# Performance work log

Hardware: AMD Instinct MI355X
Metric: run time of the kernel (lower is better)

The kernel has to match this reference:

```python
import jax, jax.numpy as jnp
import numpy as np

N_NODES = 50000
N_EDGES = 800000
IN_CH = 512
HID = 512


def setup_inputs() -> dict:
    key = jax.random.key(0)
    ks = jax.random.split(key, 8)
    x = jax.random.normal(ks[0], (N_NODES, IN_CH), dtype=jnp.float32)
    edge_index = jax.random.randint(ks[1], (2, N_EDGES), 0, N_NODES, dtype=jnp.int64)
    s_in = 1.0 / np.sqrt(IN_CH)
    s_h = 1.0 / np.sqrt(HID)
    W1 = jax.random.uniform(ks[2], (IN_CH, HID), jnp.float32, -s_in, s_in)
    b1 = jnp.zeros((HID,), jnp.float32)
    W2 = jax.random.uniform(ks[3], (HID, HID), jnp.float32, -s_h, s_h)
    b2 = jnp.zeros((HID,), jnp.float32)
    Wo = jax.random.uniform(ks[4], (HID, 1), jnp.float32, -s_h, s_h)
    bo = jnp.zeros((1,), jnp.float32)
    return {"x": x, "edge_index": edge_index, "W1": W1, "b1": b1,
            "W2": W2, "b2": b2, "Wo": Wo, "bo": bo}


def _gcn_norm(edge_index, n):
    # add self-loops, compute symmetric normalization deg^{-1/2} per edge
    loop = jnp.arange(n, dtype=edge_index.dtype)
    src = jnp.concatenate([edge_index[0], loop])  # [E+N]
    dst = jnp.concatenate([edge_index[1], loop])
    deg = jax.ops.segment_sum(jnp.ones_like(dst, dtype=jnp.float32), dst,
                              num_segments=n)
    dinv = jnp.where(deg > 0, jax.lax.rsqrt(jnp.maximum(deg, 1.0)), 0.0)
    norm = dinv[src] * dinv[dst]  # [E+N]
    return src, dst, norm


def _gcn_conv(h, src, dst, norm, W, b, n):
    h = h @ W                          # [N, H] dense GEMM first (PyG order)
    msg = h[src] * norm[:, None]       # gather + per-edge scale
    out = jax.ops.segment_sum(msg, dst, num_segments=n)  # scatter-add
    return out + b


def reference(x, edge_index, W1, b1, W2, b2, Wo, bo):
    n = x.shape[0]
    src, dst, norm = _gcn_norm(edge_index, n)
    h = jax.nn.relu(_gcn_conv(x, src, dst, norm, W1, b1, n))
    h = jax.nn.relu(_gcn_conv(h, src, dst, norm, W2, b2, n))
    logits = (h @ Wo + bo)[:, 0]       # [N]
    return jax.nn.softmax(logits, axis=0)
```

## Files before the change

### kernel.cpp

```cpp
#include <hip/hip_runtime.h>

#define NN 50000
#define NP 50176
#define NE 800000
#define CH 512
#define NB 196
#define PB_TRANS 2048
#define PB_DEG 782
#define PB_PERM 6
#define SMB 49
#define GB1 (4 * (NP / 128))
#define BKB ((NE / 2 + 255) / 256)

typedef __bf16 bf16x8 __attribute__((ext_vector_type(8)));
typedef float f32x4 __attribute__((ext_vector_type(4)));
typedef float f32x2 __attribute__((ext_vector_type(2)));
typedef unsigned short u16x8 __attribute__((ext_vector_type(8)));

static __device__ __forceinline__ unsigned short f2b(float f){
  unsigned u = __builtin_bit_cast(unsigned, f);
  u = (u + 0x7fffu + ((u >> 16) & 1u)) >> 16;
  return (unsigned short)u;
}
static __device__ __forceinline__ float b2f(unsigned short h){
  unsigned u = ((unsigned)h) << 16;
  return __builtin_bit_cast(float, u);
}
static __device__ __forceinline__ float rdlane_f(float v, int l){
  return __builtin_bit_cast(float, __builtin_amdgcn_readlane(__builtin_bit_cast(int, v), l));
}
static __device__ __forceinline__ unsigned pack2(float f0, float f1){
  unsigned u0 = __builtin_bit_cast(unsigned, f0) + 0x8000u;
  unsigned u1 = __builtin_bit_cast(unsigned, f1) + 0x8000u;
  return __builtin_amdgcn_perm(u1, u0, 0x07060302u);
}
static __device__ __forceinline__ int lam(int p){
  return (p & ~63) | (((p & 3) << 4) + ((p & 63) >> 2));
}

__global__ void k_prep(const float* __restrict__ W1, const float* __restrict__ W2,
                       unsigned short* __restrict__ W1t, unsigned short* __restrict__ W2t,
                       const int* __restrict__ ei, int* __restrict__ deg,
                       int* __restrict__ rank,
                       const float* __restrict__ b1, const float* __restrict__ b2,
                       const float* __restrict__ Wo, float* __restrict__ b1p,
                       float* __restrict__ b2p, float* __restrict__ Wop){
  const int b = blockIdx.x, t = threadIdx.x;
  if (b < PB_TRANS){
    int idx = (b & 1023) * 256 + t;
    int n = idx >> 9, p = idx & (CH - 1);
    if (b < 1024)
      W1t[n * CH + p] = f2b(W1[p * CH + n]);
    else
      W2t[n * CH + p] = f2b(W2[lam(p) * CH + n]);
  } else if (b < PB_TRANS + PB_DEG){
    int e4 = ((b - PB_TRANS) * 256 + t) * 4;
    if (e4 < NE){
      int4 d = *(const int4*)(ei + NE + e4);
      int4 r;
      r.x = atomicAdd(&deg[d.x], 1);
      r.y = atomicAdd(&deg[d.y], 1);
      r.z = atomicAdd(&deg[d.z], 1);
      r.w = atomicAdd(&deg[d.w], 1);
      *(int4*)(rank + e4) = r;
    }
  } else {
    int idx = (b - PB_TRANS - PB_DEG) * 256 + t;
    int which = idx >> 9, p = idx & (CH - 1);
    int l = lam(p);
    if (which == 0) b1p[p] = b1[l];
    else if (which == 1) b2p[p] = b2[l];
    else Wop[p] = Wo[l];
  }
}

__global__ void k_blocksum(const int* __restrict__ deg, int* __restrict__ bsum){
  __shared__ int sh[4];
  const int t = threadIdx.x;
  int i = blockIdx.x * 256 + t;
  int v = (i < NN) ? deg[i] : 0;
  #pragma unroll
  for (int off = 32; off > 0; off >>= 1) v += __shfl_down(v, off, 64);
  if ((t & 63) == 0) sh[t >> 6] = v;
  __syncthreads();
  if (t == 0) bsum[blockIdx.x] = sh[0] + sh[1] + sh[2] + sh[3];
}

__global__ void k_scatter(const int* __restrict__ deg, const int* __restrict__ bsum,
                          int* __restrict__ row_ptr, float* __restrict__ dinv){
  __shared__ int sh[256];
  __shared__ int base;
  const int t = threadIdx.x;
  int bv = (t < NB) ? bsum[t] : 0;
  sh[t] = bv; __syncthreads();
  for (int d = 1; d < 256; d <<= 1){
    int add = (t >= d) ? sh[t - d] : 0;
    __syncthreads();
    sh[t] += add;
    __syncthreads();
  }
  if (t == (int)blockIdx.x) base = sh[t] - bv;
  if (blockIdx.x == 0 && t == 255) row_ptr[NN] = sh[255];
  __syncthreads();
  const int boff0 = base;
  int i = blockIdx.x * 256 + t;
  int d0 = (i < NN) ? deg[i] : 0;
  sh[t] = d0; __syncthreads();
  for (int dd = 1; dd < 256; dd <<= 1){
    int add = (t >= dd) ? sh[t - dd] : 0;
    __syncthreads();
    sh[t] += add;
    __syncthreads();
  }
  if (i < NN){
    row_ptr[i] = sh[t] - d0 + boff0;
    dinv[i] = rsqrtf((float)d0 + 1.0f);
  }
}

template<bool CVT>
static __device__ __forceinline__ void gemm_body(
    const int bx, const int t,
    const void* __restrict__ Av, const unsigned short* __restrict__ Bt,
    unsigned char* __restrict__ C,
    unsigned short (&As)[2][8192], unsigned short (&Bs)[2][8192]){
  const int wave = t >> 6, lane = t & 63;
  const int quad = lane >> 4, l15 = lane & 15;
  const int mw = (wave & 1) * 64;
  const int nw = (wave >> 1) * 64;
  const int g = bx >> 5, rem = bx & 31;
  const int rt = g * 8 + (rem & 7);
  const int rowBase = rt * 128;
  const int nBase = (rem >> 3) * 128;

  const int lr = lane >> 2;
  const int lcs = (((lane & 3) ^ ((lr >> 1) & 3)) * 8);
  const int lr8 = lane >> 3;
  const int lc8 = lane & 7;
  const unsigned short* Bg0 = Bt + (size_t)(nBase + wave * 32 + lr) * CH + lcs;
  const int boff = wave * 1024;
  const float* X = (const float*)Av;
  const unsigned short* Ag0 = (const unsigned short*)Av;
  if (!CVT) Ag0 += (size_t)(rowBase + wave * 32 + lr) * CH + lcs;
  const int aoff = wave * 1024;

  int arow[4]; size_t asrc[4];
  int wswz = 0;
  if (CVT){
    #pragma unroll
    for (int q=0;q<4;q++){
      arow[q] = wave * 32 + q * 8 + lr8;
      int gr = rowBase + arow[q];
      if (gr >= NN) gr = 0;
      asrc[q] = (size_t)gr * CH + lc8 * 4;
    }
    wswz = (lc8 * 4) ^ ((lr8 & 6) << 2);
  }
  const int rsw = (l15 & 6) << 2;

  f32x4 acc[4][4];
  #pragma unroll
  for (int i=0;i<4;i++)
    #pragma unroll
    for (int j=0;j<4;j++) acc[i][j] = 0;

  float4 apre[2][4];

  if (CVT){
    #pragma unroll
    for (int p=0;p<2;p++)
      #pragma unroll
      for (int q=0;q<4;q++) apre[p][q] = *(const float4*)(X + asrc[q] + p*32);
    #pragma unroll
    for (int p=0;p<2;p++)
      #pragma unroll
      for (int q=0;q<4;q++){
        uint2 pk; pk.x = pack2(apre[p][q].x, apre[p][q].y);
        pk.y = pack2(apre[p][q].z, apre[p][q].w);
        *(uint2*)&As[0][p*4096 + arow[q]*32 + wswz] = pk;
      }
  } else {
    #pragma unroll
    for (int p=0;p<2;p++)
      #pragma unroll
      for (int gg=0;gg<2;gg++)
        __builtin_amdgcn_global_load_lds(
          (const __attribute__((address_space(1))) void*)(Ag0 + (size_t)gg*16*CH + p*32),
          (__attribute__((address_space(3))) void*)(&As[0][p*4096 + aoff + gg*512]), 16, 0, 0);
  }
  #pragma unroll
  for (int p=0;p<2;p++)
    #pragma unroll
    for (int gg=0;gg<2;gg++)
      __builtin_amdgcn_global_load_lds(
        (const __attribute__((address_space(1))) void*)(Bg0 + (size_t)gg*16*CH + p*32),
        (__attribute__((address_space(3))) void*)(&Bs[0][p*4096 + boff + gg*512]), 16, 0, 0);

  for (int it = 0; it < 8; it++){
    const int cur = it & 1, nxt = cur ^ 1;
    __syncthreads();
    if (it < 7){
      const int kb = (it + 1) * 64;
      if (CVT){
        #pragma unroll
        for (int p=0;p<2;p++)
          #pragma unroll
          for (int q=0;q<4;q++) apre[p][q] = *(const float4*)(X + asrc[q] + kb + p*32);
      } else {
        #pragma unroll
        for (int p=0;p<2;p++)
          #pragma unroll
          for (int gg=0;gg<2;gg++)
            __builtin_amdgcn_global_load_lds(
              (const __attribute__((address_space(1))) void*)(Ag0 + (size_t)gg*16*CH + kb + p*32),
              (__attribute__((address_space(3))) void*)(&As[nxt][p*4096 + aoff + gg*512]), 16, 0, 0);
      }
      #pragma unroll
      for (int p=0;p<2;p++)
        #pragma unroll
        for (int gg=0;gg<2;gg++)
          __builtin_amdgcn_global_load_lds(
            (const __attribute__((address_space(1))) void*)(Bg0 + (size_t)gg*16*CH + kb + p*32),
            (__attribute__((address_space(3))) void*)(&Bs[nxt][p*4096 + boff + gg*512]), 16, 0, 0);
    }

    #pragma unroll
    for (int ks=0;ks<2;ks++){
      bf16x8 af[4], bfr[4];
      #pragma unroll
      for (int i=0;i<4;i++)
        af[i] = __builtin_bit_cast(bf16x8,
                *(const u16x8*)&As[cur][ks*4096 + (mw + i*16 + l15)*32 + (quad*8 ^ rsw)]);
      #pragma unroll
      for (int j=0;j<4;j++)
        bfr[j] = __builtin_bit_cast(bf16x8,
                *(const u16x8*)&Bs[cur][ks*4096 + (nw + j*16 + l15)*32 + (quad*8 ^ rsw)]);
      #pragma unroll
      for (int i=0;i<4;i++)
        #pragma unroll
        for (int j=0;j<4;j++)
          acc[i][j] = __builtin_amdgcn_mfma_f32_16x16x32_bf16(af[i], bfr[j], acc[i][j], 0, 0, 0);
    }

    if (CVT && it < 7){
      #pragma unroll
      for (int p=0;p<2;p++)
        #pragma unroll
        for (int q=0;q<4;q++){
          uint2 pk; pk.x = pack2(apre[p][q].x, apre[p][q].y);
          pk.y = pack2(apre[p][q].z, apre[p][q].w);
          *(uint2*)&As[nxt][p*4096 + arow[q]*32 + wswz] = pk;
        }
    }
  }

  #pragma unroll
  for (int i=0;i<4;i++){
    #pragma unroll
    for (int r=0;r<4;r++){
      int row = rowBase + mw + i*16 + quad*4 + r;
      int w0 = 0;
      w0 = __builtin_amdgcn_cvt_pk_fp8_f32(acc[i][0][r], acc[i][1][r], w0, false);
      w0 = __builtin_amdgcn_cvt_pk_fp8_f32(acc[i][2][r], acc[i][3][r], w0, true);
      *(unsigned*)(C + (size_t)row * CH + nBase + nw + l15*4) = (unsigned)w0;
    }
  }
}

__launch_bounds__(256, 2)
__global__ void k_g1bkt(const float* __restrict__ x, const unsigned short* __restrict__ W1t,
                        unsigned char* __restrict__ C,
                        const int* __restrict__ ei, const int* __restrict__ row_ptr,
                        const int* __restrict__ rank, int* __restrict__ csr_src){
  __shared__ __align__(16) unsigned short As[2][8192];
  __shared__ __align__(16) unsigned short Bs[2][8192];
  const int b = blockIdx.x;
  if (b < GB1){
    gemm_body<true>(b, threadIdx.x, x, W1t, C, As, Bs);
  } else {
    int e2 = ((b - GB1) * 256 + threadIdx.x) * 2;
    if (e2 < NE){
      int2 src = *(const int2*)(ei + e2);
      int2 dst = *(const int2*)(ei + NE + e2);
      int2 rk  = *(const int2*)(rank + e2);
      csr_src[row_ptr[dst.x] + rk.x] = src.x;
      csr_src[row_ptr[dst.y] + rk.y] = src.y;
    }
  }
}

__launch_bounds__(256, 2)
__global__ void k_gemm2(const unsigned short* __restrict__ A,
                        const unsigned short* __restrict__ Bt,
                        unsigned char* __restrict__ C){
  __shared__ __align__(16) unsigned short As[2][8192];
  __shared__ __align__(16) unsigned short Bs[2][8192];
  gemm_body<false>(blockIdx.x, threadIdx.x, A, Bt, C, As, Bs);
}

template<bool HEAD>
__launch_bounds__(256)
__global__ void k_agg(const unsigned char* __restrict__ h, const int* __restrict__ row_ptr,
                      const int* __restrict__ csr_src, const float* __restrict__ dinv,
                      const float* __restrict__ bias, unsigned short* __restrict__ out,
                      const float* __restrict__ Wo, const float* __restrict__ bo,
                      float* __restrict__ logits){
  const int node = blockIdx.x * 4 + (threadIdx.x >> 6);
  const int lane = threadIdx.x & 63;
  float acc[8];
  #pragma unroll
  for (int k=0;k<8;k++) acc[k] = 0.f;
  const int rp = row_ptr[node], re = row_ptr[node + 1];
  for (int base = rp; base < re; base += 64){
    int cnt = re - base; if (cnt > 64) cnt = 64;
    int s = 0; float w = 0.f;
    if (base + lane < re){ s = csr_src[base + lane]; w = dinv[s]; }
    int j = 0;
    for (; j + 8 <= cnt; j += 8){
      int ss[8]; float ww[8]; uint2 hv[8];
      #pragma unroll
      for (int u=0;u<8;u++){
        ss[u] = __builtin_amdgcn_readlane(s, j + u);
        ww[u] = rdlane_f(w, j + u);
      }
      #pragma unroll
      for (int u=0;u<8;u++)
        hv[u] = *(const uint2*)(h + (size_t)ss[u] * CH + lane * 8);
      #pragma unroll
      for (int u=0;u<8;u++){
        f32x2 p0 = __builtin_amdgcn_cvt_pk_f32_fp8((int)hv[u].x, false);
        f32x2 p1 = __builtin_amdgcn_cvt_pk_f32_fp8((int)hv[u].x, true);
        f32x2 p2 = __builtin_amdgcn_cvt_pk_f32_fp8((int)hv[u].y, false);
        f32x2 p3 = __builtin_amdgcn_cvt_pk_f32_fp8((int)hv[u].y, true);
        acc[0] += ww[u] * p0.x; acc[1] += ww[u] * p0.y;
        acc[2] += ww[u] * p1.x; acc[3] += ww[u] * p1.y;
        acc[4] += ww[u] * p2.x; acc[5] += ww[u] * p2.y;
        acc[6] += ww[u] * p3.x; acc[7] += ww[u] * p3.y;
      }
    }
    for (; j < cnt; j++){
      int ss = __builtin_amdgcn_readlane(s, j);
      float ww = rdlane_f(w, j);
      uint2 hv = *(const uint2*)(h + (size_t)ss * CH + lane * 8);
      f32x2 p0 = __builtin_amdgcn_cvt_pk_f32_fp8((int)hv.x, false);
      f32x2 p1 = __builtin_amdgcn_cvt_pk_f32_fp8((int)hv.x, true);
      f32x2 p2 = __builtin_amdgcn_cvt_pk_f32_fp8((int)hv.y, false);
      f32x2 p3 = __builtin_amdgcn_cvt_pk_f32_fp8((int)hv.y, true);
      acc[0] += ww * p0.x; acc[1] += ww * p0.y;
      acc[2] += ww * p1.x; acc[3] += ww * p1.y;
      acc[4] += ww * p2.x; acc[5] += ww * p2.y;
      acc[6] += ww * p3.x; acc[7] += ww * p3.y;
    }
  }
  const float di = dinv[node];
  uint2 hsv = *(const uint2*)(h + (size_t)node * CH + lane * 8);
  f32x2 s0 = __builtin_amdgcn_cvt_pk_f32_fp8((int)hsv.x, false);
  f32x2 s1 = __builtin_amdgcn_cvt_pk_f32_fp8((int)hsv.x, true);
  f32x2 s2 = __builtin_amdgcn_cvt_pk_f32_fp8((int)hsv.y, false);
  f32x2 s3 = __builtin_amdgcn_cvt_pk_f32_fp8((int)hsv.y, true);
  float hsf[8] = {s0.x, s0.y, s1.x, s1.y, s2.x, s2.y, s3.x, s3.y};
  const float4* bp = (const float4*)(bias + lane * 8);
  float4 bv0 = bp[0], bv1 = bp[1];
  float bb[8] = {bv0.x,bv0.y,bv0.z,bv0.w,bv1.x,bv1.y,bv1.z,bv1.w};
  if (HEAD){
    const float4* wp = (const float4*)(Wo + lane * 8);
    float4 w0 = wp[0], w1 = wp[1];
    float wv[8] = {w0.x,w0.y,w0.z,w0.w,w1.x,w1.y,w1.z,w1.w};
    float v = 0.f;
    #pragma unroll
    for (int k=0;k<8;k++){
      float r = fmaxf(di * acc[k] + di * di * hsf[k] + bb[k], 0.f);
      v += r * wv[k];
    }
    #pragma unroll
    for (int off = 32; off > 0; off >>= 1) v += __shfl_down(v, off, 64);
    if (lane == 0) logits[node] = v + bo[0];
  } else {
    u16x8 o;
    #pragma unroll
    for (int k=0;k<8;k++){
      float r = fmaxf(di * acc[k] + di * di * hsf[k] + bb[k], 0.f);
      o[k] = f2b(r);
    }
    *(u16x8*)(out + (size_t)node * CH + lane * 8) = o;
  }
}

__global__ void k_smpart(const float* __restrict__ logits, float* __restrict__ pm,
                         float* __restrict__ ps){
  __shared__ float shm[16], shs[16];
  const int t = threadIdx.x;
  const int i = blockIdx.x * 1024 + t;
  float v = (i < NN) ? logits[i] : -3.4e38f;
  float m = v;
  #pragma unroll
  for (int off = 32; off > 0; off >>= 1) m = fmaxf(m, __shfl_down(m, off, 64));
  if ((t & 63) == 0) shm[t >> 6] = m;
  __syncthreads();
  if (t < 64){
    float mm = (t < 16) ? shm[t] : -3.4e38f;
    #pragma unroll
    for (int off = 8; off > 0; off >>= 1) mm = fmaxf(mm, __shfl_down(mm, off, 64));
    if (t == 0) shm[0] = mm;
  }
  __syncthreads();
  const float bm = shm[0];
  float s = (i < NN) ? expf(v - bm) : 0.f;
  #pragma unroll
  for (int off = 32; off > 0; off >>= 1) s += __shfl_down(s, off, 64);
  if ((t & 63) == 0) shs[t >> 6] = s;
  __syncthreads();
  if (t < 64){
    float sss = (t < 16) ? shs[t] : 0.f;
    #pragma unroll
    for (int off = 8; off > 0; off >>= 1) sss += __shfl_down(sss, off, 64);
    if (t == 0){ pm[blockIdx.x] = bm; ps[blockIdx.x] = sss; }
  }
}

__global__ void k_smwrite(const float* __restrict__ logits, const float* __restrict__ pm,
                          const float* __restrict__ ps, float* __restrict__ out){
  __shared__ float shMS[2];
  const int t = threadIdx.x;
  if (t < 64){
    float m = (t < SMB) ? pm[t] : -3.4e38f;
    float M = m;
    #pragma unroll
    for (int off = 32; off > 0; off >>= 1) M = fmaxf(M, __shfl_down(M, off, 64));
    M = rdlane_f(M, 0);
    float s = (t < SMB) ? ps[t] * expf(m - M) : 0.f;
    #pragma unroll
    for (int off = 32; off > 0; off >>= 1) s += __shfl_down(s, off, 64);
    if (t == 0){ shMS[0] = M; shMS[1] = s; }
  }
  __syncthreads();
  int i = blockIdx.x * blockDim.x + t;
  if (i < NN) out[i] = expf(logits[i] - shMS[0]) / shMS[1];
}

extern "C" void kernel_launch(void* const* d_in, const int* in_sizes, int n_in,
                              void* d_out, int out_size, void* d_ws, size_t ws_size,
                              hipStream_t stream){
  const float* x  = (const float*)d_in[0];
  const int*   ei = (const int*)d_in[1];
  const float* W1 = (const float*)d_in[2];
  const float* b1 = (const float*)d_in[3];
  const float* W2 = (const float*)d_in[4];
  const float* b2 = (const float*)d_in[5];
  const float* Wo = (const float*)d_in[6];
  const float* bo = (const float*)d_in[7];
  float* out = (float*)d_out;

  char* ws = (char*)d_ws;
  size_t off = 0;
  auto alloc = [&](size_t bytes) -> void* {
    void* p = ws + off;
    off = (off + bytes + 255) & ~(size_t)255;
    return p;
  };
  unsigned short* B0  = (unsigned short*)alloc((size_t)NP * CH * 2);
  unsigned char*  B1  = (unsigned char*)alloc((size_t)NP * CH);
  unsigned short* W1t = (unsigned short*)alloc((size_t)CH * CH * 2);
  unsigned short* W2t = (unsigned short*)alloc((size_t)CH * CH * 2);
  int*   deg     = (int*)alloc((size_t)NN * 4);
  float* dinv    = (float*)alloc((size_t)NN * 4);
  int*   row_ptr = (int*)alloc((size_t)(NN + 1) * 4);
  int*   rank    = (int*)alloc((size_t)NE * 4);
  int*   csr     = (int*)alloc((size_t)NE * 4);
  float* logits  = (float*)alloc((size_t)NN * 4);
  int*   bsum    = (int*)alloc((size_t)NB * 4);
  float* pm      = (float*)alloc((size_t)SMB * 4);
  float* ps      = (float*)alloc((size_t)SMB * 4);
  float* b1p     = (float*)alloc((size_t)CH * 4);
  float* b2p     = (float*)alloc((size_t)CH * 4);
  float* Wop     = (float*)alloc((size_t)CH * 4);

  hipMemsetAsync(deg, 0, (size_t)NN * 4, stream);
  k_prep<<<PB_TRANS + PB_DEG + PB_PERM, 256, 0, stream>>>(
      W1, W2, W1t, W2t, ei, deg, rank, b1, b2, Wo, b1p, b2p, Wop);
  k_blocksum<<<NB, 256, 0, stream>>>(deg, bsum);
  k_scatter<<<NB, 256, 0, stream>>>(deg, bsum, row_ptr, dinv);

  k_g1bkt<<<GB1 + BKB, 256, 0, stream>>>(x, W1t, B1, ei, row_ptr, rank, csr);
  k_agg<false><<<NN / 4, 256, 0, stream>>>(B1, row_ptr, csr, dinv, b1p, B0,
                                           Wop, bo, logits);
  k_gemm2<<<GB1, 256, 0, stream>>>(B0, W2t, B1);
  k_agg<true><<<NN / 4, 256, 0, stream>>>(B1, row_ptr, csr, dinv, b2p, B0,
                                          Wop, bo, logits);

  k_smpart<<<SMB, 1024, 0, stream>>>(logits, pm, ps);
  k_smwrite<<<NB, 256, 0, stream>>>(logits, pm, ps, out);
}
```

Measured before the change: 422.9 us.

## Slice feature matrices into 64-channel planes and aggregate per slice

Stores the GEMM outputs and the intermediate activations as eight 64-channel planes (NP x 64 each) instead of row-major 512-wide rows. The aggregation kernel then splits channels across 8 blocks per node group, with each wave processing 8 edges in parallel using 8 lanes per edge and reducing with xor shuffles. The intent is to shrink the gathered working set per plane so it fits better in cache and to raise memory-level parallelism. The cost is atomics on the logits, which need an extra memset, more blocks, and shuffle reductions.

```diff
diff --git a/kernel.cpp b/kernel.cpp
--- a/kernel.cpp
+++ b/kernel.cpp
@@ -11,6 +11,7 @@
 #define SMB 49
 #define GB1 (4 * (NP / 128))
 #define BKB ((NE / 2 + 255) / 256)
+#define AGB (8 * (NN / 16))
 
 typedef __bf16 bf16x8 __attribute__((ext_vector_type(8)));
 typedef float f32x4 __attribute__((ext_vector_type(4)));
@@ -21,10 +22,6 @@
   unsigned u = __builtin_bit_cast(unsigned, f);
   u = (u + 0x7fffu + ((u >> 16) & 1u)) >> 16;
   return (unsigned short)u;
-}
-static __device__ __forceinline__ float b2f(unsigned short h){
-  unsigned u = ((unsigned)h) << 16;
-  return __builtin_bit_cast(float, u);
 }
 static __device__ __forceinline__ float rdlane_f(float v, int l){
   return __builtin_bit_cast(float, __builtin_amdgcn_readlane(__builtin_bit_cast(int, v), l));
@@ -141,7 +138,7 @@
   const int boff = wave * 1024;
   const float* X = (const float*)Av;
   const unsigned short* Ag0 = (const unsigned short*)Av;
-  if (!CVT) Ag0 += (size_t)(rowBase + wave * 32 + lr) * CH + lcs;
+  if (!CVT) Ag0 += (size_t)(rowBase + wave * 32 + lr) * 64 + lcs;
   const int aoff = wave * 1024;
 
   int arow[4]; size_t asrc[4];
@@ -185,7 +182,7 @@
       #pragma unroll
       for (int gg=0;gg<2;gg++)
         __builtin_amdgcn_global_load_lds(
-          (const __attribute__((address_space(1))) void*)(Ag0 + (size_t)gg*16*CH + p*32),
+          (const __attribute__((address_space(1))) void*)(Ag0 + (size_t)gg*1024 + p*32),
           (__attribute__((address_space(3))) void*)(&As[0][p*4096 + aoff + gg*512]), 16, 0, 0);
   }
   #pragma unroll
@@ -207,12 +204,13 @@
           #pragma unroll
           for (int q=0;q<4;q++) apre[p][q] = *(const float4*)(X + asrc[q] + kb + p*32);
       } else {
+        const size_t apl = (size_t)(it + 1) * ((size_t)NP * 64);
         #pragma unroll
         for (int p=0;p<2;p++)
           #pragma unroll
           for (int gg=0;gg<2;gg++)
             __builtin_amdgcn_global_load_lds(
-              (const __attribute__((address_space(1))) void*)(Ag0 + (size_t)gg*16*CH + kb + p*32),
+              (const __attribute__((address_space(1))) void*)(Ag0 + apl + (size_t)gg*1024 + p*32),
               (__attribute__((address_space(3))) void*)(&As[nxt][p*4096 + aoff + gg*512]), 16, 0, 0);
       }
       #pragma unroll
@@ -254,6 +252,8 @@
     }
   }
 
+  const int sl = (nBase + nw) >> 6;
+  unsigned char* Cb = C + (size_t)sl * ((size_t)NP * 64);
   #pragma unroll
   for (int i=0;i<4;i++){
     #pragma unroll
@@ -262,7 +262,7 @@
       int w0 = 0;
       w0 = __builtin_amdgcn_cvt_pk_fp8_f32(acc[i][0][r], acc[i][1][r], w0, false);
       w0 = __builtin_amdgcn_cvt_pk_fp8_f32(acc[i][2][r], acc[i][3][r], w0, true);
-      *(unsigned*)(C + (size_t)row * CH + nBase + nw + l15*4) = (unsigned)w0;
+      *(unsigned*)(Cb + (size_t)row * 64 + l15*4) = (unsigned)w0;
     }
   }
 }
@@ -305,84 +305,81 @@
                       const float* __restrict__ bias, unsigned short* __restrict__ out,
                       const float* __restrict__ Wo, const float* __restrict__ bo,
                       float* __restrict__ logits){
-  const int node = blockIdx.x * 4 + (threadIdx.x >> 6);
-  const int lane = threadIdx.x & 63;
-  float acc[8];
-  #pragma unroll
-  for (int k=0;k<8;k++) acc[k] = 0.f;
-  const int rp = row_ptr[node], re = row_ptr[node + 1];
-  for (int base = rp; base < re; base += 64){
-    int cnt = re - base; if (cnt > 64) cnt = 64;
-    int s = 0; float w = 0.f;
-    if (base + lane < re){ s = csr_src[base + lane]; w = dinv[s]; }
-    int j = 0;
-    for (; j + 8 <= cnt; j += 8){
-      int ss[8]; float ww[8]; uint2 hv[8];
-      #pragma unroll
-      for (int u=0;u<8;u++){
-        ss[u] = __builtin_amdgcn_readlane(s, j + u);
-        ww[u] = rdlane_f(w, j + u);
-      }
-      #pragma unroll
-      for (int u=0;u<8;u++)
-        hv[u] = *(const uint2*)(h + (size_t)ss[u] * CH + lane * 8);
-      #pragma unroll
-      for (int u=0;u<8;u++){
-        f32x2 p0 = __builtin_amdgcn_cvt_pk_f32_fp8((int)hv[u].x, false);
-        f32x2 p1 = __builtin_amdgcn_cvt_pk_f32_fp8((int)hv[u].x, true);
-        f32x2 p2 = __builtin_amdgcn_cvt_pk_f32_fp8((int)hv[u].y, false);
-        f32x2 p3 = __builtin_amdgcn_cvt_pk_f32_fp8((int)hv[u].y, true);
-        acc[0] += ww[u] * p0.x; acc[1] += ww[u] * p0.y;
-        acc[2] += ww[u] * p1.x; acc[3] += ww[u] * p1.y;
-        acc[4] += ww[u] * p2.x; acc[5] += ww[u] * p2.y;
-        acc[6] += ww[u] * p3.x; acc[7] += ww[u] * p3.y;
-      }
-    }
-    for (; j < cnt; j++){
-      int ss = __builtin_amdgcn_readlane(s, j);
-      float ww = rdlane_f(w, j);
-      uint2 hv = *(const uint2*)(h + (size_t)ss * CH + lane * 8);
+  const int s    = blockIdx.x & 7;
+  const int grp  = blockIdx.x >> 3;
+  const int wave = threadIdx.x >> 6, lane = threadIdx.x & 63;
+  const int eg   = lane >> 3;
+  const int ch8  = lane & 7;
+  const unsigned char* hs = h + (size_t)s * ((size_t)NP * 64);
+
+  const float4* bp = (const float4*)(bias + s*64 + ch8*8);
+  float4 bv0 = bp[0], bv1 = bp[1];
+  float bb[8] = {bv0.x,bv0.y,bv0.z,bv0.w,bv1.x,bv1.y,bv1.z,bv1.w};
+  float wv[8];
+  if (HEAD){
+    const float4* wp = (const float4*)(Wo + s*64 + ch8*8);
+    float4 w0 = wp[0], w1 = wp[1];
+    wv[0]=w0.x; wv[1]=w0.y; wv[2]=w0.z; wv[3]=w0.w;
+    wv[4]=w1.x; wv[5]=w1.y; wv[6]=w1.z; wv[7]=w1.w;
+  }
+
+  #pragma unroll 1
+  for (int i = 0; i < 4; i++){
+    const int n = grp * 16 + wave * 4 + i;
+    if (n >= NN) break;
+    const int rp = row_ptr[n], re = row_ptr[n + 1];
+    float acc[8];
+    #pragma unroll
+    for (int k=0;k<8;k++) acc[k] = 0.f;
+    for (int base = rp; base < re; base += 8){
+      int ei = base + eg;
+      int src = 0; float w = 0.f;
+      if (ei < re){ src = csr_src[ei]; w = dinv[src]; }
+      uint2 hv = *(const uint2*)(hs + (size_t)src * 64 + ch8 * 8);
       f32x2 p0 = __builtin_amdgcn_cvt_pk_f32_fp8((int)hv.x, false);
       f32x2 p1 = __builtin_amdgcn_cvt_pk_f32_fp8((int)hv.x, true);
       f32x2 p2 = __builtin_amdgcn_cvt_pk_f32_fp8((int)hv.y, false);
       f32x2 p3 = __builtin_amdgcn_cvt_pk_f32_fp8((int)hv.y, true);
-      acc[0] += ww * p0.x; acc[1] += ww * p0.y;
-      acc[2] += ww * p1.x; acc[3] += ww * p1.y;
-      acc[4] += ww * p2.x; acc[5] += ww * p2.y;
-      acc[6] += ww * p3.x; acc[7] += ww * p3.y;
-    }
-  }
-  const float di = dinv[node];
-  uint2 hsv = *(const uint2*)(h + (size_t)node * CH + lane * 8);
-  f32x2 s0 = __builtin_amdgcn_cvt_pk_f32_fp8((int)hsv.x, false);
-  f32x2 s1 = __builtin_amdgcn_cvt_pk_f32_fp8((int)hsv.x, true);
-  f32x2 s2 = __builtin_amdgcn_cvt_pk_f32_fp8((int)hsv.y, false);
-  f32x2 s3 = __builtin_amdgcn_cvt_pk_f32_fp8((int)hsv.y, true);
-  float hsf[8] = {s0.x, s0.y, s1.x, s1.y, s2.x, s2.y, s3.x, s3.y};
-  const float4* bp = (const float4*)(bias + lane * 8);
-  float4 bv0 = bp[0], bv1 = bp[1];
-  float bb[8] = {bv0.x,bv0.y,bv0.z,bv0.w,bv1.x,bv1.y,bv1.z,bv1.w};
-  if (HEAD){
-    const float4* wp = (const float4*)(Wo + lane * 8);
-    float4 w0 = wp[0], w1 = wp[1];
-    float wv[8] = {w0.x,w0.y,w0.z,w0.w,w1.x,w1.y,w1.z,w1.w};
-    float v = 0.f;
-    #pragma unroll
-    for (int k=0;k<8;k++){
-      float r = fmaxf(di * acc[k] + di * di * hsf[k] + bb[k], 0.f);
-      v += r * wv[k];
-    }
-    #pragma unroll
-    for (int off = 32; off > 0; off >>= 1) v += __shfl_down(v, off, 64);
-    if (lane == 0) logits[node] = v + bo[0];
-  } else {
-    u16x8 o;
-    #pragma unroll
-    for (int k=0;k<8;k++){
-      float r = fmaxf(di * acc[k] + di * di * hsf[k] + bb[k], 0.f);
-      o[k] = f2b(r);
-    }
-    *(u16x8*)(out + (size_t)node * CH + lane * 8) = o;
+      acc[0] += w * p0.x; acc[1] += w * p0.y;
+      acc[2] += w * p1.x; acc[3] += w * p1.y;
+      acc[4] += w * p2.x; acc[5] += w * p2.y;
+      acc[6] += w * p3.x; acc[7] += w * p3.y;
+    }
+    #pragma unroll
+    for (int m = 8; m <= 32; m <<= 1)
+      #pragma unroll
+      for (int k=0;k<8;k++) acc[k] += __shfl_xor(acc[k], m, 64);
+
+    const float di = dinv[n];
+    uint2 hsv = *(const uint2*)(hs + (size_t)n * 64 + ch8 * 8);
+    f32x2 s0 = __builtin_amdgcn_cvt_pk_f32_fp8((int)hsv.x, false);
+    f32x2 s1 = __builtin_amdgcn_cvt_pk_f32_fp8((int)hsv.x, true);
+    f32x2 s2 = __builtin_amdgcn_cvt_pk_f32_fp8((int)hsv.y, false);
+    f32x2 s3 = __builtin_amdgcn_cvt_pk_f32_fp8((int)hsv.y, true);
+    float hsf[8] = {s0.x, s0.y, s1.x, s1.y, s2.x, s2.y, s3.x, s3.y};
+
+    if (HEAD){
+      float v = 0.f;
+      #pragma unroll
+      for (int k=0;k<8;k++){
+        float r = fmaxf(di * acc[k] + di * di * hsf[k] + bb[k], 0.f);
+        v += r * wv[k];
+      }
+      v += __shfl_xor(v, 1, 64);
+      v += __shfl_xor(v, 2, 64);
+      v += __shfl_xor(v, 4, 64);
+      if (lane == 0) atomicAdd(&logits[n], (s == 0) ? v + bo[0] : v);
+    } else {
+      if (eg == 0){
+        u16x8 o;
+        #pragma unroll
+        for (int k=0;k<8;k++){
+          float r = fmaxf(di * acc[k] + di * di * hsf[k] + bb[k], 0.f);
+          o[k] = f2b(r);
+        }
+        *(u16x8*)(out + (size_t)s * ((size_t)NP * 64) + (size_t)n * 64 + ch8 * 8) = o;
+      }
+    }
   }
 }
 
@@ -476,17 +473,18 @@
   float* Wop     = (float*)alloc((size_t)CH * 4);
 
   hipMemsetAsync(deg, 0, (size_t)NN * 4, stream);
+  hipMemsetAsync(logits, 0, (size_t)NN * 4, stream);
   k_prep<<<PB_TRANS + PB_DEG + PB_PERM, 256, 0, stream>>>(
       W1, W2, W1t, W2t, ei, deg, rank, b1, b2, Wo, b1p, b2p, Wop);
   k_blocksum<<<NB, 256, 0, stream>>>(deg, bsum);
   k_scatter<<<NB, 256, 0, stream>>>(deg, bsum, row_ptr, dinv);
 
   k_g1bkt<<<GB1 + BKB, 256, 0, stream>>>(x, W1t, B1, ei, row_ptr, rank, csr);
-  k_agg<false><<<NN / 4, 256, 0, stream>>>(B1, row_ptr, csr, dinv, b1p, B0,
-                                           Wop, bo, logits);
+  k_agg<false><<<AGB, 256, 0, stream>>>(B1, row_ptr, csr, dinv, b1p, B0,
+                                        Wop, bo, logits);
   k_gemm2<<<GB1, 256, 0, stream>>>(B0, W2t, B1);
-  k_agg<true><<<NN / 4, 256, 0, stream>>>(B1, row_ptr, csr, dinv, b2p, B0,
-                                          Wop, bo, logits);
+  k_agg<true><<<AGB, 256, 0, stream>>>(B1, row_ptr, csr, dinv, b2p, B0,
+                                       Wop, bo, logits);
 
   k_smpart<<<SMB, 1024, 0, stream>>>(logits, pm, ps);
   k_smwrite<<<NB, 256, 0, stream>>>(logits, pm, ps, out);
```

After: 612.8 us. +44.9%, slower.
